# Kernel optimization log

Hardware: AMD Instinct MI355X
Metric: run time of the kernel (lower is better)

The kernel has to match this reference:

```python
import jax, jax.numpy as jnp
import numpy as np

IMG = 128          # img_size
P = 8              # patch_size
H = 768            # model dim (hidden_size)
E = 1536           # GAU expansion dim (2*H), u/v width
K = 128            # key_size
L = (IMG // P) ** 2   # 256 patches
PD = P * P * 3        # 192 patch dim
T = 1000
NL = 24


def sinusoidal_embeddings(pos, dim, base):
    # pos: (L,) -> (L, dim) = [sin | cos]
    half = dim // 2
    freqs = jnp.exp(jnp.arange(half, dtype=jnp.float32) * (-np.log(base) / (half - 1)))
    ang = pos[:, None].astype(jnp.float32) * freqs[None, :]
    return jnp.concatenate([jnp.sin(ang), jnp.cos(ang)], axis=-1)


def make_rope_2d():
    w = IMG // P
    pos = jnp.arange(w * w)
    emb1 = sinusoidal_embeddings(pos // w, 64, 1000.0)
    emb2 = sinusoidal_embeddings(pos % w, 64, 1000.0)
    return jnp.concatenate([emb1, emb2], axis=-1)[None]  # (1, L, 128)


def apply_rope(x, pe):
    # faithful to source: sin_emb = pe[..., :d/2], cos_emb = pe[..., d/2:]
    d = pe.shape[-1]
    sin = pe[..., : d // 2]
    cos = pe[..., d // 2 :]
    x1 = x[..., : d // 2]
    x2 = x[..., d // 2 : d]
    return jnp.concatenate([x1 * cos - x2 * sin, x2 * cos + x1 * sin], axis=-1)


def rmsnorm(x, w):
    rms = jnp.sqrt(jnp.mean(x * x, axis=-1, keepdims=True))
    return x / (rms + 1e-6) * w


def setup_inputs() -> dict:
    key = jax.random.key(0)
    ks = jax.random.split(key, 9)
    B = 16
    s = 0.02
    return {
        "x": jax.random.normal(ks[0], (B, 3, IMG, IMG), dtype=jnp.float32),
        "t_idx": jax.random.randint(ks[1], (B, 1), 0, T),
        "patch_W": jax.random.normal(ks[2], (PD, H), dtype=jnp.float32) * s,
        "t_emb": jax.random.normal(ks[3], (T, H), dtype=jnp.float32) * s,
        "Wuv": jax.random.normal(ks[4], (NL, H, 2 * E + 2 * K), dtype=jnp.float32) * s,
        "Wout": jax.random.normal(ks[5], (NL, E, H), dtype=jnp.float32) * s,
        "gnorm": jnp.ones((NL, H), dtype=jnp.float32),
        "fnorm_w": jnp.ones((H,), dtype=jnp.float32),
        "unpatch_W": jax.random.normal(ks[6], (H, PD), dtype=jnp.float32) * s,
    }


def reference(x, t_idx, patch_W, t_emb, Wuv, Wout, gnorm, fnorm_w, unpatch_W):
    B = x.shape[0]
    g = IMG // P
    # patchify: (B,3,128,128) -> (B, 256, 192)
    xp = x.reshape(B, 3, g, P, g, P).transpose(0, 2, 4, 3, 5, 1).reshape(B, L, PD)
    h = xp @ patch_W + t_emb[t_idx[:, 0]][:, None, :]   # (B, L, H)
    pe = make_rope_2d()                                  # (1, L, 128)
    scale = K ** (-0.5)

    def block(h, params):
        wuv, wout, gn = params
        xn = rmsnorm(h, gn)
        uvqk = xn @ wuv                                  # (B, L, 2E+2K)
        u = jax.nn.silu(uvqk[..., :E])
        v = jax.nn.silu(uvqk[..., E : 2 * E])
        q = apply_rope(uvqk[..., 2 * E : 2 * E + K], pe)
        k = apply_rope(uvqk[..., 2 * E + K :], pe)
        attn = jax.nn.softmax(jnp.einsum('blk,bmk->blm', q, k) * scale, axis=-1)
        o = u * jnp.einsum('blm,bme->ble', attn, v)      # (B, L, E)
        return h + o @ wout, None

    h, _ = jax.lax.scan(block, h, (Wuv, Wout, gnorm))
    h = rmsnorm(h, fnorm_w) @ unpatch_W                  # (B, L, PD)
    # unpatchify: (B,256,192) -> (B,3,128,128)
    out = h.reshape(B, g, g, P, P, 3).transpose(0, 5, 1, 3, 2, 4).reshape(B, 3, IMG, IMG)
    return out
```

## Files before the change

### kernel.cpp

```cpp
#include <hip/hip_runtime.h>
#include <math.h>

#define IMG   128
#define Hdim  768
#define Edim  1536
#define Ltok  256
#define PDim  192
#define NLAY  24
#define Bsz   16
#define Mrows 4096
#define UVW   3328

typedef __bf16 bf16x8 __attribute__((ext_vector_type(8)));
typedef float  f32x4  __attribute__((ext_vector_type(4)));

__device__ __forceinline__ unsigned short f2b(float f) {
    unsigned int u = __float_as_uint(f);
    unsigned int r = (u + 0x7FFF + ((u >> 16) & 1)) >> 16;
    return (unsigned short)r;
}
__device__ __forceinline__ float b2f(unsigned short s) {
    return __uint_as_float((unsigned int)s << 16);
}
__device__ __forceinline__ unsigned int pk2(float lo, float hi) {
    return (unsigned int)f2b(lo) | ((unsigned int)f2b(hi) << 16);
}
__device__ __forceinline__ float silu(float x) {
    return x / (1.0f + expf(-x));
}
__device__ __forceinline__ void gload16(const void* g, void* l) {
    __builtin_amdgcn_global_load_lds(
        (const __attribute__((address_space(1))) void*)g,
        (__attribute__((address_space(3))) void*)l, 16, 0, 0);
}
__device__ __forceinline__ int xcd_wg() {
    int nwg = gridDim.x;
    int orig = blockIdx.x;
    int q8 = nwg >> 3, r8 = nwg & 7;
    int xcd = orig & 7, loc = orig >> 3;
    return (xcd < r8 ? xcd * (q8 + 1) : r8 * (q8 + 1) + (xcd - r8) * q8) + loc;
}

__global__ void pe_kernel(float* __restrict__ pe) {
    int l = blockIdx.x;
    int j = threadIdx.x;
    const float c = -logf(1000.0f) / 31.0f;
    int   sub = j & 31;
    float f   = expf(c * (float)sub);
    float pos = (j < 64) ? (float)(l >> 4) : (float)(l & 15);
    float ang = pos * f;
    pe[l * 128 + j] = ((j & 32) == 0) ? sinf(ang) : cosf(ang);
}

__global__ void patchify_kernel(const float* __restrict__ x, unsigned short* __restrict__ xp) {
    int bc = blockIdx.x;
    int iy = bc & 127;
    int t  = bc >> 7;
    int c  = t % 3;
    int b  = t / 3;
    int ix = threadIdx.x;
    float v = x[((size_t)(b * 3 + c) * IMG + iy) * IMG + ix];
    int gy = iy >> 3, py = iy & 7, gx = ix >> 3, px = ix & 7;
    xp[(size_t)(b * Ltok + gy * 16 + gx) * PDim + (py * 8 + px) * 3 + c] = f2b(v);
}

__global__ void trans_kernel(const float* __restrict__ src, int ldS, long long sS,
                             unsigned short* __restrict__ dst, int ldD, long long sD) {
    src += (long long)blockIdx.z * sS;
    dst += (long long)blockIdx.z * sD;
    __shared__ float t[32][33];
    int c0 = blockIdx.x * 32, r0 = blockIdx.y * 32;
    int tx = threadIdx.x, ty = threadIdx.y;
#pragma unroll
    for (int i = 0; i < 4; ++i)
        t[ty + 8 * i][tx] = src[(size_t)(r0 + ty + 8 * i) * ldS + c0 + tx];
    __syncthreads();
#pragma unroll
    for (int i = 0; i < 4; ++i)
        dst[(size_t)(c0 + ty + 8 * i) * ldD + r0 + tx] = f2b(t[tx][ty + 8 * i]);
}

template <int ACC>
__launch_bounds__(256)
__global__ void gemm_bf16(const unsigned short* __restrict__ A, int lda,
                          const unsigned short* __restrict__ Bt, int ldb,
                          float* __restrict__ C, int ldc,
                          int Kt, int Nt, int nbx) {
    __shared__ unsigned short lsA[2][4096];
    __shared__ unsigned short lsB[2][4096];
    int wg = xcd_wg();
    int bx = wg % nbx, by = wg / nbx;
    int tid  = threadIdx.x;
    int lane = tid & 63, w = tid >> 6, wr = w >> 1, wc = w & 1;
    int row0 = by * 128, col0 = bx * 128;
    int fr = lane & 15, fk = (lane >> 4) * 8;
    f32x4 acc[4][4] = {};

    int c0 = tid, c1 = tid + 256;
    int ar0 = row0 + (c0 >> 2), ar1 = row0 + (c1 >> 2);
    int bn0 = col0 + (c0 >> 2), bn1 = col0 + (c1 >> 2);
    if (bn0 > Nt - 1) bn0 = Nt - 1;
    if (bn1 > Nt - 1) bn1 = Nt - 1;
    int ka0 = (c0 & 3) * 8, ka1 = (c1 & 3) * 8;

#define STAGE_G(buf, k0)                                                       \
    gload16(A  + (size_t)ar0 * lda + (k0) + ka0, &lsA[buf][c0 * 8]);           \
    gload16(A  + (size_t)ar1 * lda + (k0) + ka1, &lsA[buf][c1 * 8]);           \
    gload16(Bt + (size_t)bn0 * ldb + (k0) + ka0, &lsB[buf][c0 * 8]);           \
    gload16(Bt + (size_t)bn1 * ldb + (k0) + ka1, &lsB[buf][c1 * 8]);

    STAGE_G(0, 0);
    __syncthreads();
    int nt = Kt >> 5, cur = 0;
    for (int t = 0; t < nt; ++t) {
        if (t + 1 < nt) { STAGE_G(cur ^ 1, (t + 1) * 32); }
        bf16x8 af[4], bfr[4];
#pragma unroll
        for (int m = 0; m < 4; ++m)
            af[m] = *(const bf16x8*)(&lsA[cur][(wr * 64 + m * 16 + fr) * 32 + fk]);
#pragma unroll
        for (int n = 0; n < 4; ++n)
            bfr[n] = *(const bf16x8*)(&lsB[cur][(wc * 64 + n * 16 + fr) * 32 + fk]);
#pragma unroll
        for (int m = 0; m < 4; ++m)
#pragma unroll
            for (int n = 0; n < 4; ++n)
                acc[m][n] = __builtin_amdgcn_mfma_f32_16x16x32_bf16(af[m], bfr[n], acc[m][n], 0, 0, 0);
        __syncthreads();
        cur ^= 1;
    }
#undef STAGE_G

    int crow = (lane >> 4) * 4;
#pragma unroll
    for (int m = 0; m < 4; ++m) {
#pragma unroll
        for (int n = 0; n < 4; ++n) {
            int gc = col0 + wc * 64 + n * 16 + fr;
            if (gc >= Nt) continue;
#pragma unroll
            for (int j = 0; j < 4; ++j) {
                size_t idx = (size_t)(row0 + wr * 64 + m * 16 + crow + j) * ldc + gc;
                if (ACC) C[idx] += acc[m][n][j];
                else     C[idx]  = acc[m][n][j];
            }
        }
    }
}

__launch_bounds__(256)
__global__ void gemm_wout(const unsigned short* __restrict__ A,
                          const unsigned short* __restrict__ Bt,
                          float* __restrict__ P) {
    __shared__ unsigned short lsA[2][4096];
    __shared__ unsigned short lsB[2][4096];
    int wg = xcd_wg();
    int sk = wg / 192, rem = wg % 192;
    int bx = rem % 6, by = rem / 6;
    int koff = sk * 768;
    float* C = P + (size_t)sk * Mrows * Hdim;
    int tid  = threadIdx.x;
    int lane = tid & 63, w = tid >> 6, wr = w >> 1, wc = w & 1;
    int row0 = by * 128, col0 = bx * 128;
    int fr = lane & 15, fk = (lane >> 4) * 8;
    f32x4 acc[4][4] = {};

    int c0 = tid, c1 = tid + 256;
    int ar0 = row0 + (c0 >> 2), ar1 = row0 + (c1 >> 2);
    int bn0 = col0 + (c0 >> 2), bn1 = col0 + (c1 >> 2);
    int ka0 = koff + (c0 & 3) * 8, ka1 = koff + (c1 & 3) * 8;

#define STAGE_W(buf, k0)                                                       \
    gload16(A  + (size_t)ar0 * Edim + (k0) + ka0, &lsA[buf][c0 * 8]);          \
    gload16(A  + (size_t)ar1 * Edim + (k0) + ka1, &lsA[buf][c1 * 8]);          \
    gload16(Bt + (size_t)bn0 * Edim + (k0) + ka0, &lsB[buf][c0 * 8]);          \
    gload16(Bt + (size_t)bn1 * Edim + (k0) + ka1, &lsB[buf][c1 * 8]);

    STAGE_W(0, 0);
    __syncthreads();
    int cur = 0;
    for (int t = 0; t < 24; ++t) {
        if (t + 1 < 24) { STAGE_W(cur ^ 1, (t + 1) * 32); }
        bf16x8 af[4], bfr[4];
#pragma unroll
        for (int m = 0; m < 4; ++m)
            af[m] = *(const bf16x8*)(&lsA[cur][(wr * 64 + m * 16 + fr) * 32 + fk]);
#pragma unroll
        for (int n = 0; n < 4; ++n)
            bfr[n] = *(const bf16x8*)(&lsB[cur][(wc * 64 + n * 16 + fr) * 32 + fk]);
#pragma unroll
        for (int m = 0; m < 4; ++m)
#pragma unroll
            for (int n = 0; n < 4; ++n)
                acc[m][n] = __builtin_amdgcn_mfma_f32_16x16x32_bf16(af[m], bfr[n], acc[m][n], 0, 0, 0);
        __syncthreads();
        cur ^= 1;
    }
#undef STAGE_W

    int crow = (lane >> 4) * 4;
#pragma unroll
    for (int m = 0; m < 4; ++m) {
#pragma unroll
        for (int n = 0; n < 4; ++n) {
            int gc = col0 + wc * 64 + n * 16 + fr;
#pragma unroll
            for (int j = 0; j < 4; ++j)
                C[(size_t)(row0 + wr * 64 + m * 16 + crow + j) * Hdim + gc] = acc[m][n][j];
        }
    }
}

__global__ __launch_bounds__(512, 2)
void gemm_uvqk8(const unsigned short* __restrict__ A,
                const unsigned short* __restrict__ Bt,
                unsigned short* __restrict__ uT,
                unsigned short* __restrict__ vT,
                unsigned short* __restrict__ qh,
                unsigned short* __restrict__ kh,
                const float* __restrict__ pe) {
    __shared__ char smem[131072];
    int wg = xcd_wg();
    int bx = wg % 13, by = wg / 13;
    int tid = threadIdx.x, lane = tid & 63, wid = tid >> 6;
    int wm = wid >> 2, wn = wid & 3;
    int row0 = by * 256, col0 = bx * 256;
    int fr = lane & 15, hi = lane >> 4;
    f32x4 acc[8][4] = {};

    int d0 = tid * 16, d1 = d0 + 8192;
    int s0 = d0 ^ (((d0 >> 7) & 7) << 4);
    int s1 = d1 ^ (((d1 >> 7) & 7) << 4);
    int sr0 = s0 >> 7, sc0 = (s0 & 127) >> 1;
    int sr1 = s1 >> 7, sc1 = (s1 & 127) >> 1;

#define STG_A(bufo, h, kt) do {                                                            \
    gload16(A + (size_t)(row0 + (h) * 128 + sr0) * Hdim + (kt) * 64 + sc0,                 \
            smem + (bufo) + (h) * 16384 + d0);                                             \
    gload16(A + (size_t)(row0 + (h) * 128 + sr1) * Hdim + (kt) * 64 + sc1,                 \
            smem + (bufo) + (h) * 16384 + d1); } while (0)
#define STG_B(bufo, h, kt) do {                                                            \
    gload16(Bt + (size_t)(col0 + (h) * 128 + sr0) * Hdim + (kt) * 64 + sc0,                \
            smem + (bufo) + 32768 + (h) * 16384 + d0);                                     \
    gload16(Bt + (size_t)(col0 + (h) * 128 + sr1) * Hdim + (kt) * 64 + sc1,                \
            smem + (bufo) + 32768 + (h) * 16384 + d1); } while (0)

    int axor = (fr & 7) << 4;
    int abase = wm * 16384 + fr * 128;
    int bbase = 32768 + (wn >> 1) * 16384 + ((wn & 1) * 64 + fr) * 128;
    int koff0 = (hi * 16) ^ axor;
    int koff1 = (hi * 16 + 64) ^ axor;

    STG_A(0, 0, 0); STG_A(0, 1, 0); STG_B(0, 0, 0); STG_B(0, 1, 0);
    STG_A(65536, 0, 1); STG_A(65536, 1, 1);
    asm volatile("s_waitcnt vmcnt(4)" ::: "memory");
    __builtin_amdgcn_s_barrier();
    __builtin_amdgcn_sched_barrier(0);

    bf16x8 af[4][2], bf0[2][2], bf1[2][2];
    const int NKT = Hdim / 64;
    for (int kt = 0; kt < NKT; ++kt) {
        int curo = (kt & 1) << 16, nxto = curo ^ 65536;
        const char* bufc = smem + curo;

#pragma unroll
        for (int m = 0; m < 4; ++m) {
            af[m][0] = *(const bf16x8*)(bufc + abase + m * 2048 + koff0);
            af[m][1] = *(const bf16x8*)(bufc + abase + m * 2048 + koff1);
        }
#pragma unroll
        for (int n = 0; n < 2; ++n) {
            bf0[n][0] = *(const bf16x8*)(bufc + bbase + n * 2048 + koff0);
            bf0[n][1] = *(const bf16x8*)(bufc + bbase + n * 2048 + koff1);
        }
        if (kt + 1 < NKT) STG_B(nxto, 0, kt + 1);
        __builtin_amdgcn_s_setprio(1);
#pragma unroll
        for (int m = 0; m < 4; ++m)
#pragma unroll
            for (int n = 0; n < 2; ++n) {
                acc[m][n] = __builtin_amdgcn_mfma_f32_16x16x32_bf16(af[m][0], bf0[n][0], acc[m][n], 0, 0, 0);
                acc[m][n] = __builtin_amdgcn_mfma_f32_16x16x32_bf16(af[m][1], bf0[n][1], acc[m][n], 0, 0, 0);
            }
        __builtin_amdgcn_s_setprio(0);
        __builtin_amdgcn_s_barrier();
        __builtin_amdgcn_sched_barrier(0);

#pragma unroll
        for (int n = 0; n < 2; ++n) {
            bf1[n][0] = *(const bf16x8*)(bufc + bbase + (n + 2) * 2048 + koff0);
            bf1[n][1] = *(const bf16x8*)(bufc + bbase + (n + 2) * 2048 + koff1);
        }
        if (kt + 1 < NKT) STG_B(nxto, 1, kt + 1);
        __builtin_amdgcn_s_setprio(1);
#pragma unroll
        for (int m = 0; m < 4; ++m)
#pragma unroll
            for (int n = 0; n < 2; ++n) {
                acc[m][n + 2] = __builtin_amdgcn_mfma_f32_16x16x32_bf16(af[m][0], bf1[n][0], acc[m][n + 2], 0, 0, 0);
                acc[m][n + 2] = __builtin_amdgcn_mfma_f32_16x16x32_bf16(af[m][1], bf1[n][1], acc[m][n + 2], 0, 0, 0);
            }
        __builtin_amdgcn_s_setprio(0);
        __builtin_amdgcn_s_barrier();
        __builtin_amdgcn_sched_barrier(0);

#pragma unroll
        for (int m = 0; m < 4; ++m) {
            af[m][0] = *(const bf16x8*)(bufc + abase + (m + 4) * 2048 + koff0);
            af[m][1] = *(const bf16x8*)(bufc + abase + (m + 4) * 2048 + koff1);
        }
        __builtin_amdgcn_s_setprio(1);
#pragma unroll
        for (int m = 0; m < 4; ++m)
#pragma unroll
            for (int n = 0; n < 2; ++n) {
                acc[m + 4][n] = __builtin_amdgcn_mfma_f32_16x16x32_bf16(af[m][0], bf0[n][0], acc[m + 4][n], 0, 0, 0);
                acc[m + 4][n] = __builtin_amdgcn_mfma_f32_16x16x32_bf16(af[m][1], bf0[n][1], acc[m + 4][n], 0, 0, 0);
            }
        __builtin_amdgcn_s_setprio(0);
        __builtin_amdgcn_s_barrier();
        __builtin_amdgcn_sched_barrier(0);

        if (kt + 2 < NKT) { STG_A(curo, 0, kt + 2); STG_A(curo, 1, kt + 2); }
        __builtin_amdgcn_s_setprio(1);
#pragma unroll
        for (int m = 0; m < 4; ++m)
#pragma unroll
            for (int n = 0; n < 2; ++n) {
                acc[m + 4][n + 2] = __builtin_amdgcn_mfma_f32_16x16x32_bf16(af[m][0], bf1[n][0], acc[m + 4][n + 2], 0, 0, 0);
                acc[m + 4][n + 2] = __builtin_amdgcn_mfma_f32_16x16x32_bf16(af[m][1], bf1[n][1], acc[m + 4][n + 2], 0, 0, 0);
            }
        __builtin_amdgcn_s_setprio(0);
        asm volatile("s_waitcnt vmcnt(4)" ::: "memory");
        __builtin_amdgcn_s_barrier();
        __builtin_amdgcn_sched_barrier(0);
    }
#undef STG_A
#undef STG_B

    if (bx == 12) {
        float* S = (float*)smem;
        const float qscale = 0.08838834764831845f;
#pragma unroll
        for (int p = 0; p < 4; ++p) {
            __syncthreads();
            if (wm == (p >> 1)) {
#pragma unroll
                for (int m = 0; m < 4; ++m) {
                    int mf = (p & 1) * 4 + m;
                    int rl = m * 16 + hi * 4;
#pragma unroll
                    for (int n = 0; n < 4; ++n) {
                        int cl = wn * 64 + n * 16 + fr;
#pragma unroll
                        for (int j = 0; j < 4; ++j)
                            S[(rl + j) * 256 + cl] = acc[mf][n][j];
                    }
                }
            }
            __syncthreads();
            int r = tid >> 3;
            int dbase = (tid & 7) * 8;
            int row_g = row0 + p * 64 + r;
            int l = row_g & 255;
#pragma unroll
            for (int i = 0; i < 8; ++i) {
                int d = dbase + i;
                float sn = pe[l * 128 + d], cs = pe[l * 128 + 64 + d];
                float q1 = S[r * 256 + d],       q2 = S[r * 256 + d + 64];
                float k1 = S[r * 256 + d + 128], k2 = S[r * 256 + d + 192];
                qh[(size_t)row_g * 128 + d]      = f2b((q1 * cs - q2 * sn) * qscale);
                qh[(size_t)row_g * 128 + d + 64] = f2b((q2 * cs + q1 * sn) * qscale);
                kh[(size_t)row_g * 128 + d]      = f2b(k1 * cs - k2 * sn);
                kh[(size_t)row_g * 128 + d + 64] = f2b(k2 * cs + k1 * sn);
            }
        }
        return;
    }

#pragma unroll
    for (int mf = 0; mf < 8; ++mf) {
        int row = row0 + wm * 128 + mf * 16 + hi * 4;
#pragma unroll
        for (int nf = 0; nf < 4; ++nf) {
            int gc = col0 + wn * 64 + nf * 16 + fr;
            ushort4 pk;
            pk.x = f2b(silu(acc[mf][nf][0]));
            pk.y = f2b(silu(acc[mf][nf][1]));
            pk.z = f2b(silu(acc[mf][nf][2]));
            pk.w = f2b(silu(acc[mf][nf][3]));
            if (bx < 6) {
                *(ushort4*)(uT + (size_t)gc * Mrows + row) = pk;
            } else {
                int e = gc - Edim;
                int b = row >> 8, l = row & 255;
                *(ushort4*)(vT + ((size_t)b * Edim + e) * Ltok + l) = pk;
            }
        }
    }
}

__launch_bounds__(256)
__global__ void fused_attn(const unsigned short* __restrict__ qh,
                           const unsigned short* __restrict__ kh,
                           const unsigned short* __restrict__ vT,
                           const unsigned short* __restrict__ uT,
                           unsigned short* __restrict__ ob) {
    int ec = blockIdx.x, qt = blockIdx.y, b = blockIdx.z;
    int tid  = threadIdx.x;
    int lane = tid & 63, w = tid >> 6;
    int fr = lane & 15, hi = lane >> 4;
    int qbase = b * 256 + qt * 64 + w * 16;

    bf16x8 qf[4];
#pragma unroll
    for (int ks = 0; ks < 4; ++ks)
        qf[ks] = *(const bf16x8*)(qh + (size_t)(qbase + fr) * 128 + ks * 32 + hi * 8);
    f32x4 sacc[16] = {};
#pragma unroll
    for (int mf = 0; mf < 16; ++mf) {
#pragma unroll
        for (int ks = 0; ks < 4; ++ks) {
            bf16x8 kf = *(const bf16x8*)(kh + (size_t)(b * 256 + mf * 16 + fr) * 128 + ks * 32 + hi * 8);
            sacc[mf] = __builtin_amdgcn_mfma_f32_16x16x32_bf16(kf, qf[ks], sacc[mf], 0, 0, 0);
        }
    }

    float mx = -3.4e38f;
#pragma unroll
    for (int mf = 0; mf < 16; ++mf)
#pragma unroll
        for (int j = 0; j < 4; ++j)
            mx = fmaxf(mx, sacc[mf][j]);
    mx = fmaxf(mx, __shfl_xor(mx, 16, 64));
    mx = fmaxf(mx, __shfl_xor(mx, 32, 64));
    float sum = 0.f;
#pragma unroll
    for (int mf = 0; mf < 16; ++mf)
#pragma unroll
        for (int j = 0; j < 4; ++j) {
            float e = expf(sacc[mf][j] - mx);
            sacc[mf][j] = e;
            sum += e;
        }
    sum += __shfl_xor(sum, 16, 64);
    sum += __shfl_xor(sum, 32, 64);
    float inv = 1.0f / sum;

    unsigned int dw[16][2];
#pragma unroll
    for (int mf = 0; mf < 16; ++mf) {
        dw[mf][0] = pk2(sacc[mf][0] * inv, sacc[mf][1] * inv);
        dw[mf][1] = pk2(sacc[mf][2] * inv, sacc[mf][3] * inv);
    }

    int sA = fr + 32 * (hi & 1);
    int sB = sA + 16;
    bool up = (hi >> 1) != 0;
    unsigned int pa[8][4];
#pragma unroll
    for (int ks = 0; ks < 8; ++ks) {
        unsigned int a00 = __shfl((int)dw[2 * ks][0],     sA, 64);
        unsigned int a01 = __shfl((int)dw[2 * ks + 1][0], sA, 64);
        unsigned int a10 = __shfl((int)dw[2 * ks][1],     sA, 64);
        unsigned int a11 = __shfl((int)dw[2 * ks + 1][1], sA, 64);
        unsigned int b00 = __shfl((int)dw[2 * ks][0],     sB, 64);
        unsigned int b01 = __shfl((int)dw[2 * ks + 1][0], sB, 64);
        unsigned int b10 = __shfl((int)dw[2 * ks][1],     sB, 64);
        unsigned int b11 = __shfl((int)dw[2 * ks + 1][1], sB, 64);
        pa[ks][0] = up ? a01 : a00;
        pa[ks][1] = up ? a11 : a10;
        pa[ks][2] = up ? b01 : b00;
        pa[ks][3] = up ? b11 : b10;
    }

    const unsigned short* vb = vT + (size_t)b * Edim * Ltok;
    int e0 = ec * 192;
#pragma unroll 2
    for (int ef = 0; ef < 12; ++ef) {
        int e = e0 + ef * 16 + fr;
        f32x4 oacc = {};
#pragma unroll
        for (int ks = 0; ks < 8; ++ks) {
            bf16x8 vf = *(const bf16x8*)(vb + (size_t)e * Ltok + ks * 32 + hi * 8);
            oacc = __builtin_amdgcn_mfma_f32_16x16x32_bf16(*(const bf16x8*)&pa[ks], vf, oacc, 0, 0, 0);
        }
        ushort4 uv = *(const ushort4*)(uT + (size_t)e * Mrows + qbase + hi * 4);
        ob[(size_t)(qbase + hi * 4 + 0) * Edim + e] = f2b(oacc[0] * b2f(uv.x));
        ob[(size_t)(qbase + hi * 4 + 1) * Edim + e] = f2b(oacc[1] * b2f(uv.y));
        ob[(size_t)(qbase + hi * 4 + 2) * Edim + e] = f2b(oacc[2] * b2f(uv.z));
        ob[(size_t)(qbase + hi * 4 + 3) * Edim + e] = f2b(oacc[3] * b2f(uv.w));
    }
}

__global__ void bias_kernel(float* __restrict__ h, const float* __restrict__ t_emb,
                            const int* __restrict__ t_idx) {
    int r = blockIdx.x;
    int b = r >> 8;
    const float* e = t_emb + (size_t)t_idx[b] * Hdim;
    float* hr = h + (size_t)r * Hdim;
    for (int i = threadIdx.x; i < Hdim; i += 256) hr[i] += e[i];
}

template <int ADD>
__global__ void rmsnorm_kernel(float* __restrict__ x, const float* __restrict__ p,
                               const float* __restrict__ w, unsigned short* __restrict__ y) {
    int r = blockIdx.x * 4 + (threadIdx.x >> 6);
    int lane = threadIdx.x & 63;
    float* xr = x + (size_t)r * Hdim;
    float4 a = *(const float4*)&xr[lane * 4];
    float4 b = *(const float4*)&xr[lane * 4 + 256];
    float4 c = *(const float4*)&xr[lane * 4 + 512];
    if (ADD) {
        const float* p0 = p + (size_t)r * Hdim;
        const float* p1 = p + (size_t)(Mrows + r) * Hdim;
        float4 a0 = *(const float4*)&p0[lane * 4];
        float4 b0 = *(const float4*)&p0[lane * 4 + 256];
        float4 c0 = *(const float4*)&p0[lane * 4 + 512];
        float4 a1 = *(const float4*)&p1[lane * 4];
        float4 b1 = *(const float4*)&p1[lane * 4 + 256];
        float4 c1 = *(const float4*)&p1[lane * 4 + 512];
        a.x += a0.x + a1.x; a.y += a0.y + a1.y; a.z += a0.z + a1.z; a.w += a0.w + a1.w;
        b.x += b0.x + b1.x; b.y += b0.y + b1.y; b.z += b0.z + b1.z; b.w += b0.w + b1.w;
        c.x += c0.x + c1.x; c.y += c0.y + c1.y; c.z += c0.z + c1.z; c.w += c0.w + c1.w;
        *(float4*)&xr[lane * 4]       = a;
        *(float4*)&xr[lane * 4 + 256] = b;
        *(float4*)&xr[lane * 4 + 512] = c;
    }
    float ss = a.x * a.x + a.y * a.y + a.z * a.z + a.w * a.w
             + b.x * b.x + b.y * b.y + b.z * b.z + b.w * b.w
             + c.x * c.x + c.y * c.y + c.z * c.z + c.w * c.w;
#pragma unroll
    for (int o = 1; o < 64; o <<= 1) ss += __shfl_xor(ss, o, 64);
    float s = 1.0f / (sqrtf(ss / (float)Hdim) + 1e-6f);
    float4 wa = *(const float4*)&w[lane * 4];
    float4 wb = *(const float4*)&w[lane * 4 + 256];
    float4 wc = *(const float4*)&w[lane * 4 + 512];
    unsigned short* yr = y + (size_t)r * Hdim;
    ushort4 o0, o1, o2;
    o0.x = f2b(a.x * s * wa.x); o0.y = f2b(a.y * s * wa.y);
    o0.z = f2b(a.z * s * wa.z); o0.w = f2b(a.w * s * wa.w);
    o1.x = f2b(b.x * s * wb.x); o1.y = f2b(b.y * s * wb.y);
    o1.z = f2b(b.z * s * wb.z); o1.w = f2b(b.w * s * wb.w);
    o2.x = f2b(c.x * s * wc.x); o2.y = f2b(c.y * s * wc.y);
    o2.z = f2b(c.z * s * wc.z); o2.w = f2b(c.w * s * wc.w);
    *(ushort4*)&yr[lane * 4]       = o0;
    *(ushort4*)&yr[lane * 4 + 256] = o1;
    *(ushort4*)&yr[lane * 4 + 512] = o2;
}

__global__ void unpatch_kernel(const float* __restrict__ y, float* __restrict__ out) {
    int bc = blockIdx.x;
    int iy = bc & 127;
    int t  = bc >> 7;
    int c  = t % 3;
    int b  = t / 3;
    int ix = threadIdx.x;
    int gy = iy >> 3, py = iy & 7, gx = ix >> 3, px = ix & 7;
    out[((size_t)(b * 3 + c) * IMG + iy) * IMG + ix] =
        y[(size_t)(b * Ltok + gy * 16 + gx) * PDim + (py * 8 + px) * 3 + c];
}

extern "C" void kernel_launch(void* const* d_in, const int* in_sizes, int n_in,
                              void* d_out, int out_size, void* d_ws, size_t ws_size,
                              hipStream_t stream) {
    const float* x        = (const float*)d_in[0];
    const int*   t_idx    = (const int*)  d_in[1];
    const float* patch_W  = (const float*)d_in[2];
    const float* t_emb    = (const float*)d_in[3];
    const float* Wuv      = (const float*)d_in[4];
    const float* Wout     = (const float*)d_in[5];
    const float* gnorm    = (const float*)d_in[6];
    const float* fnorm    = (const float*)d_in[7];
    const float* unpatchW = (const float*)d_in[8];
    float* out = (float*)d_out;

    char* wsb = (char*)d_ws;
    size_t off = 0;
    auto alloc = [&](size_t bytes) { char* p = wsb + off; off += (bytes + 255) & ~(size_t)255; return p; };
    float* pe   = (float*)alloc(256 * 128 * 4);
    float* h    = (float*)alloc((size_t)Mrows * Hdim * 4);
    float* pbuf = (float*)alloc((size_t)2 * Mrows * Hdim * 4);
    float* y    = (float*)alloc((size_t)Mrows * PDim * 4);
    unsigned short* xp   = (unsigned short*)alloc((size_t)Mrows * PDim * 2);
    unsigned short* xn   = (unsigned short*)alloc((size_t)Mrows * Hdim * 2);
    unsigned short* uT   = (unsigned short*)alloc((size_t)Edim * Mrows * 2);
    unsigned short* vT   = (unsigned short*)alloc((size_t)Bsz * Edim * Ltok * 2);
    unsigned short* qh   = (unsigned short*)alloc((size_t)Mrows * 128 * 2);
    unsigned short* kh   = (unsigned short*)alloc((size_t)Mrows * 128 * 2);
    unsigned short* o_bf = (unsigned short*)alloc((size_t)Mrows * Edim * 2);
    unsigned short* WuvT  = (unsigned short*)alloc((size_t)NLAY * UVW * Hdim * 2);
    unsigned short* WoutT = (unsigned short*)alloc((size_t)NLAY * Hdim * Edim * 2);
    unsigned short* patchWT   = (unsigned short*)alloc((size_t)Hdim * PDim * 2);
    unsigned short* unpatchWT = (unsigned short*)alloc((size_t)PDim * Hdim * 2);
    if (off > ws_size) return;

    pe_kernel<<<256, 128, 0, stream>>>(pe);
    patchify_kernel<<<Bsz * 3 * IMG, IMG, 0, stream>>>(x, xp);

    trans_kernel<<<dim3(Hdim / 32, PDim / 32, 1), dim3(32, 8), 0, stream>>>(
        patch_W, Hdim, 0, patchWT, PDim, 0);
    trans_kernel<<<dim3(PDim / 32, Hdim / 32, 1), dim3(32, 8), 0, stream>>>(
        unpatchW, PDim, 0, unpatchWT, Hdim, 0);
    trans_kernel<<<dim3(UVW / 32, Hdim / 32, NLAY), dim3(32, 8), 0, stream>>>(
        Wuv, UVW, (long long)Hdim * UVW, WuvT, Hdim, (long long)UVW * Hdim);
    trans_kernel<<<dim3(Hdim / 32, Edim / 32, NLAY), dim3(32, 8), 0, stream>>>(
        Wout, Hdim, (long long)Edim * Hdim, WoutT, Edim, (long long)Hdim * Edim);

    gemm_bf16<0><<<(Hdim / 128) * (Mrows / 128), 256, 0, stream>>>(
        xp, PDim, patchWT, PDim, h, Hdim, PDim, Hdim, Hdim / 128);
    bias_kernel<<<Mrows, 256, 0, stream>>>(h, t_emb, t_idx);

    rmsnorm_kernel<0><<<Mrows / 4, 256, 0, stream>>>(h, nullptr, gnorm, xn);
    for (int l = 0; l < NLAY; ++l) {
        gemm_uvqk8<<<13 * (Mrows / 256), 512, 0, stream>>>(
            xn, WuvT + (size_t)l * UVW * Hdim, uT, vT, qh, kh, pe);
        fused_attn<<<dim3(8, 4, Bsz), 256, 0, stream>>>(qh, kh, vT, uT, o_bf);
        gemm_wout<<<384, 256, 0, stream>>>(
            o_bf, WoutT + (size_t)l * Hdim * Edim, pbuf);
        const float* nw = (l + 1 < NLAY) ? gnorm + (size_t)(l + 1) * Hdim : fnorm;
        rmsnorm_kernel<1><<<Mrows / 4, 256, 0, stream>>>(h, pbuf, nw, xn);
    }

    gemm_bf16<0><<<2 * (Mrows / 128), 256, 0, stream>>>(
        xn, Hdim, unpatchWT, Hdim, y, PDim, Hdim, PDim, 2);
    unpatch_kernel<<<Bsz * 3 * IMG, IMG, 0, stream>>>(y, out);
}
```

Before: 2.997 ms.

## Stage uvqk epilogue through LDS for coalesced stores; split-K Wout into four

The u/v epilogue of the uvqk GEMM now writes its activated tile into shared memory with an XOR swizzle. It then writes transposed rows back to global memory as contiguous 16-byte chunks instead of scattered 8-byte stores. Separately, the output-projection GEMM goes from split-K of 2 to split-K of 4, launching 768 workgroups with half the K loop each. The RMSNorm then reduces four partial buffers, which costs more partial-sum memory traffic and a larger workspace in exchange for more parallelism.

```diff
diff --git a/kernel.cpp b/kernel.cpp
--- a/kernel.cpp
+++ b/kernel.cpp
@@ -157,7 +157,7 @@
     int wg = xcd_wg();
     int sk = wg / 192, rem = wg % 192;
     int bx = rem % 6, by = rem / 6;
-    int koff = sk * 768;
+    int koff = sk * 384;
     float* C = P + (size_t)sk * Mrows * Hdim;
     int tid  = threadIdx.x;
     int lane = tid & 63, w = tid >> 6, wr = w >> 1, wc = w & 1;
@@ -179,8 +179,8 @@
     STAGE_W(0, 0);
     __syncthreads();
     int cur = 0;
-    for (int t = 0; t < 24; ++t) {
-        if (t + 1 < 24) { STAGE_W(cur ^ 1, (t + 1) * 32); }
+    for (int t = 0; t < 12; ++t) {
+        if (t + 1 < 12) { STAGE_W(cur ^ 1, (t + 1) * 32); }
         bf16x8 af[4], bfr[4];
 #pragma unroll
         for (int m = 0; m < 4; ++m)
@@ -378,25 +378,38 @@
         return;
     }
 
+    __syncthreads();
 #pragma unroll
     for (int mf = 0; mf < 8; ++mf) {
-        int row = row0 + wm * 128 + mf * 16 + hi * 4;
+        int m_l = wm * 128 + mf * 16 + hi * 4;
 #pragma unroll
         for (int nf = 0; nf < 4; ++nf) {
-            int gc = col0 + wn * 64 + nf * 16 + fr;
+            int e_l = wn * 64 + nf * 16 + fr;
             ushort4 pk;
             pk.x = f2b(silu(acc[mf][nf][0]));
             pk.y = f2b(silu(acc[mf][nf][1]));
             pk.z = f2b(silu(acc[mf][nf][2]));
             pk.w = f2b(silu(acc[mf][nf][3]));
-            if (bx < 6) {
-                *(ushort4*)(uT + (size_t)gc * Mrows + row) = pk;
-            } else {
-                int e = gc - Edim;
-                int b = row >> 8, l = row & 255;
-                *(ushort4*)(vT + ((size_t)b * Edim + e) * Ltok + l) = pk;
-            }
-        }
+            int byte = (e_l * 512 + m_l * 2) ^ ((e_l & 7) << 4);
+            *(ushort4*)(smem + byte) = pk;
+        }
+    }
+    __syncthreads();
+    int er = tid >> 5;
+    int ch = (tid & 31) * 16;
+#pragma unroll
+    for (int it = 0; it < 16; ++it) {
+        int e_l = it * 16 + er;
+        int byte = (e_l * 512 + ch) ^ ((e_l & 7) << 4);
+        int4 v = *(const int4*)(smem + byte);
+        unsigned short* dst;
+        if (bx < 6) {
+            dst = uT + (size_t)(col0 + e_l) * Mrows + row0;
+        } else {
+            int e = col0 + e_l - Edim;
+            dst = vT + ((size_t)(row0 >> 8) * Edim + e) * Ltok;
+        }
+        *(int4*)((char*)dst + ch) = v;
     }
 }
 
@@ -512,17 +525,16 @@
     float4 b = *(const float4*)&xr[lane * 4 + 256];
     float4 c = *(const float4*)&xr[lane * 4 + 512];
     if (ADD) {
-        const float* p0 = p + (size_t)r * Hdim;
-        const float* p1 = p + (size_t)(Mrows + r) * Hdim;
-        float4 a0 = *(const float4*)&p0[lane * 4];
-        float4 b0 = *(const float4*)&p0[lane * 4 + 256];
-        float4 c0 = *(const float4*)&p0[lane * 4 + 512];
-        float4 a1 = *(const float4*)&p1[lane * 4];
-        float4 b1 = *(const float4*)&p1[lane * 4 + 256];
-        float4 c1 = *(const float4*)&p1[lane * 4 + 512];
-        a.x += a0.x + a1.x; a.y += a0.y + a1.y; a.z += a0.z + a1.z; a.w += a0.w + a1.w;
-        b.x += b0.x + b1.x; b.y += b0.y + b1.y; b.z += b0.z + b1.z; b.w += b0.w + b1.w;
-        c.x += c0.x + c1.x; c.y += c0.y + c1.y; c.z += c0.z + c1.z; c.w += c0.w + c1.w;
+#pragma unroll
+        for (int s = 0; s < 4; ++s) {
+            const float* ps = p + (size_t)(s * Mrows + r) * Hdim;
+            float4 a0 = *(const float4*)&ps[lane * 4];
+            float4 b0 = *(const float4*)&ps[lane * 4 + 256];
+            float4 c0 = *(const float4*)&ps[lane * 4 + 512];
+            a.x += a0.x; a.y += a0.y; a.z += a0.z; a.w += a0.w;
+            b.x += b0.x; b.y += b0.y; b.z += b0.z; b.w += b0.w;
+            c.x += c0.x; c.y += c0.y; c.z += c0.z; c.w += c0.w;
+        }
         *(float4*)&xr[lane * 4]       = a;
         *(float4*)&xr[lane * 4 + 256] = b;
         *(float4*)&xr[lane * 4 + 512] = c;
@@ -580,7 +592,7 @@
     auto alloc = [&](size_t bytes) { char* p = wsb + off; off += (bytes + 255) & ~(size_t)255; return p; };
     float* pe   = (float*)alloc(256 * 128 * 4);
     float* h    = (float*)alloc((size_t)Mrows * Hdim * 4);
-    float* pbuf = (float*)alloc((size_t)2 * Mrows * Hdim * 4);
+    float* pbuf = (float*)alloc((size_t)4 * Mrows * Hdim * 4);
     float* y    = (float*)alloc((size_t)Mrows * PDim * 4);
     unsigned short* xp   = (unsigned short*)alloc((size_t)Mrows * PDim * 2);
     unsigned short* xn   = (unsigned short*)alloc((size_t)Mrows * Hdim * 2);
@@ -616,7 +628,7 @@
         gemm_uvqk8<<<13 * (Mrows / 256), 512, 0, stream>>>(
             xn, WuvT + (size_t)l * UVW * Hdim, uT, vT, qh, kh, pe);
         fused_attn<<<dim3(8, 4, Bsz), 256, 0, stream>>>(qh, kh, vT, uT, o_bf);
-        gemm_wout<<<384, 256, 0, stream>>>(
+        gemm_wout<<<768, 256, 0, stream>>>(
             o_bf, WoutT + (size_t)l * Hdim * Edim, pbuf);
         const float* nw = (l + 1 < NLAY) ? gnorm + (size_t)(l + 1) * Hdim : fnorm;
         rmsnorm_kernel<1><<<Mrows / 4, 256, 0, stream>>>(h, pbuf, nw, xn);
```

Measured after the change: 2.821 ms. 1.06x faster.
